# Performance work log

Measured on AMD Instinct MI355X. Metric: run time of the kernel, lower is better.

Reference implementation:

```python
import jax, jax.numpy as jnp
import numpy as np

N, D_IN, D_HID, D_OUT, E = 100000, 128, 256, 64, 1600000


def setup_inputs() -> dict:
    key = jax.random.key(0)
    ks = jax.random.split(key, 6)
    x = jax.random.normal(ks[0], (N, D_IN), dtype=jnp.float32)
    edge_index = jax.random.randint(ks[1], (2, E), 0, N, dtype=jnp.int64)
    # Linear params (PyTorch convention: y = x @ W.T + b)
    W1 = jax.random.normal(ks[2], (D_HID, D_IN), dtype=jnp.float32) / np.sqrt(D_IN)
    b1 = jax.random.normal(ks[3], (D_HID,), dtype=jnp.float32) * 0.01
    W2 = jax.random.normal(ks[4], (D_OUT, D_HID), dtype=jnp.float32) / np.sqrt(D_HID)
    b2 = jax.random.normal(ks[5], (D_OUT,), dtype=jnp.float32) * 0.01
    return {"x": x, "edge_index": edge_index, "W1": W1, "b1": b1, "W2": W2, "b2": b2}


def _scatter_mean(vals, dst, num_nodes):
    # sum neighbor features per destination node, divide by in-degree (0-degree -> 0)
    s = jax.ops.segment_sum(vals, dst, num_segments=num_nodes)
    cnt = jax.ops.segment_sum(jnp.ones((dst.shape[0],), vals.dtype), dst, num_segments=num_nodes)
    return s / jnp.maximum(cnt, 1.0)[:, None]


def _sage_layer(x, src, dst, W, b):
    neighbors = x[src]                      # [E, d] gather
    agg = _scatter_mean(neighbors, dst, x.shape[0])  # [N, d]
    return agg @ W.T + b


def reference(x, edge_index, W1, b1, W2, b2):
    src, dst = edge_index[0], edge_index[1]
    h = _sage_layer(x, src, dst, W1, b1)
    h = jax.nn.relu(h)
    # dropout is identity at inference (training=False)
    y = _sage_layer(h, src, dst, W2, b2)
    return jax.nn.log_softmax(y, axis=1)
```

## Files before the change

### kernel.cpp

```cpp
#include <hip/hip_runtime.h>


typedef __attribute__((ext_vector_type(8))) short bf16x8;
typedef __attribute__((ext_vector_type(4))) float f32x4;
typedef __attribute__((ext_vector_type(2))) float f32x2;

#define BSHIFT 10
#define BMASK  1023
#define SRCMASK 0x1FFFF
#define TBIN   4096

#if __has_builtin(__builtin_amdgcn_cvt_pk_f32_fp8) && __has_builtin(__builtin_amdgcn_cvt_pk_fp8_f32)
#define HAVE_FP8_CVT 1
#else
#define HAVE_FP8_CVT 0
#endif

__device__ inline ushort f2bf(float f) {
  union { float f; unsigned u; } c; c.f = f;
  unsigned r = (c.u + 0x7fffu + ((c.u >> 16) & 1u)) >> 16;
  return (ushort)r;
}
__device__ inline float bf2f(ushort u) {
  union { unsigned u; float f; } c; c.u = ((unsigned)u) << 16;
  return c.f;
}

#if HAVE_FP8_CVT
template <bool HI>
__device__ inline f32x2 fp8x2f(unsigned w) {
  return __builtin_amdgcn_cvt_pk_f32_fp8((int)w, HI);
}
template <bool HI>
__device__ inline unsigned fp8pack2(unsigned old, float a, float b) {
  return (unsigned)__builtin_amdgcn_cvt_pk_fp8_f32(a, b, (int)old, HI);
}
#else
__device__ inline float fp8tof_1(unsigned b) {
  unsigned e = (b >> 3) & 15u, m = b & 7u;
  float v;
  if (e == 0) v = (float)m * 0x1p-9f;
  else { union { unsigned u; float f; } c; c.u = ((e + 120u) << 23) | (m << 20); v = c.f; }
  return (b & 0x80u) ? -v : v;
}
template <bool HI>
__device__ inline f32x2 fp8x2f(unsigned w) {
  unsigned sh = HI ? 16 : 0;
  f32x2 r;
  r.x = fp8tof_1((w >> sh) & 0xFFu);
  r.y = fp8tof_1((w >> (sh + 8)) & 0xFFu);
  return r;
}
__device__ inline unsigned f2fp8_1(float f) {
  float af = fabsf(f);
  unsigned s = (f < 0.f) ? 0x80u : 0u;
  if (!(af < 448.f)) return s | 0x7Eu;
  if (af < 0x1p-6f) {
    int m = (int)rintf(af * 512.0f);
    if (m >= 8) return s | 0x08u;
    return s | (unsigned)m;
  }
  int e;
  frexpf(af, &e);
  int E = e - 1;
  int q = (int)rintf(ldexpf(af, 3 - E));
  if (q >= 16) { q = 8; E += 1; if (E > 8) return s | 0x7Eu; }
  return s | ((unsigned)(E + 7) << 3) | ((unsigned)q & 7u);
}
template <bool HI>
__device__ inline unsigned fp8pack2(unsigned old, float a, float b) {
  unsigned pair = f2fp8_1(a) | (f2fp8_1(b) << 8);
  return HI ? ((old & 0x0000FFFFu) | (pair << 16)) : ((old & 0xFFFF0000u) | pair);
}
#endif

__global__ void __launch_bounds__(64) k_detect(const int* __restrict__ ei, int* __restrict__ flag) {
  int t = threadIdx.x;
  int v = ei[2 * t + 1];
  unsigned long long m = __ballot(v != 0);
  if (t == 0) *flag = (m == 0ull) ? 1 : 0;
}

__global__ void __launch_bounds__(256) k_prep_x(const float4* __restrict__ x4, uint2* __restrict__ xq8, int total8) {
  int i = blockIdx.x * 256 + threadIdx.x;
  if (i >= total8) return;
  float4 v0 = x4[2 * i], v1 = x4[2 * i + 1];
  unsigned w0 = fp8pack2<false>(0u, v0.x, v0.y);
  w0 = fp8pack2<true>(w0, v0.z, v0.w);
  unsigned w1 = fp8pack2<false>(0u, v1.x, v1.y);
  w1 = fp8pack2<true>(w1, v1.z, v1.w);
  xq8[i] = make_uint2(w0, w1);
}

__global__ void __launch_bounds__(256) k_prep_w(const float* __restrict__ W1, const float* __restrict__ W2,
                                                ushort* __restrict__ W1f, ushort* __restrict__ W2f) {
  int idx = blockIdx.x * 256 + threadIdx.x;
  if (idx < 32768) {
    int jt = idx >> 11, rem = idx & 2047;
    int kt = rem >> 9, rem2 = rem & 511;
    int l = rem2 >> 3, e = rem2 & 7;
    int k = kt * 32 + (l >> 4) * 8 + e;
    int j = jt * 16 + (l & 15);
    W1f[idx] = f2bf(W1[j * 128 + k]);
  } else {
    int i2 = idx - 32768;
    if (i2 < 16384) {
      int ot = i2 >> 12, rem = i2 & 4095;
      int kt = rem >> 9;
      int l = (rem >> 3) & 63, e = rem & 7;
      int k = kt * 32 + (l >> 4) * 8 + e;
      int o = ot * 16 + (l & 15);
      W2f[i2] = f2bf(W2[o * 256 + k]);
    }
  }
}

__global__ void __launch_bounds__(256) k_bhist(const int* __restrict__ ei, const int* __restrict__ flag,
                                               int* __restrict__ bcnt, int E, int NB) {
  __shared__ int h[128];
  int t = threadIdx.x;
  if (t < 128) h[t] = 0;
  __syncthreads();
  bool f64 = (*flag != 0);
  int stride = gridDim.x * 256;
  for (int e = blockIdx.x * 256 + t; e < E; e += stride) {
    int d;
    if (f64) d = (int)((const long long*)ei)[(size_t)E + e];
    else     d = ei[(size_t)E + e];
    atomicAdd(&h[d >> BSHIFT], 1);
  }
  __syncthreads();
  if (t < NB && h[t]) atomicAdd(&bcnt[t], h[t]);
}

__global__ void __launch_bounds__(128) k_bscan(const int* __restrict__ bcnt, int* __restrict__ bbase,
                                               int* __restrict__ bcur, int* __restrict__ row_ptr,
                                               int NB, int N, int E) {
  __shared__ int s[128];
  int t = threadIdx.x;
  int v = (t < NB) ? bcnt[t] : 0;
  s[t] = v;
  __syncthreads();
  for (int o = 1; o < 128; o <<= 1) {
    int u = (t >= o) ? s[t - o] : 0;
    __syncthreads();
    s[t] += u;
    __syncthreads();
  }
  if (t < NB) {
    int base = s[t] - v;
    bbase[t] = base;
    bcur[t] = base;
  }
  if (t == 0) {
    bbase[NB] = E;
    row_ptr[N] = E;
  }
}

__global__ void __launch_bounds__(256) k_bin(const int* __restrict__ ei, const int* __restrict__ flag,
                                             int* __restrict__ bcur, int* __restrict__ gpair, int E, int NB) {
  __shared__ int hist[128], base[128], segb[128], cur[128], scanb[128];
  __shared__ int ent[TBIN];
  __shared__ int gdx[TBIN];
  int t = threadIdx.x;
  int e0 = blockIdx.x * TBIN;
  int cnt = E - e0; if (cnt > TBIN) cnt = TBIN;
  if (t < 128) hist[t] = 0;
  __syncthreads();
  bool f64 = (*flag != 0);
  int ment[16], mbk[16];
#pragma unroll
  for (int i = 0; i < 16; ++i) {
    int idx = t + i * 256;
    mbk[i] = -1;
    if (idx < cnt) {
      int e = e0 + idx;
      int s, d;
      if (f64) {
        const long long* p = (const long long*)ei;
        s = (int)p[e];
        d = (int)p[(size_t)E + e];
      } else {
        s = ei[e];
        d = ei[(size_t)E + e];
      }
      int b = d >> BSHIFT;
      mbk[i] = b;
      ment[i] = ((d & BMASK) << 17) | s;
      atomicAdd(&hist[b], 1);
    }
  }
  __syncthreads();
  if (t < 128) scanb[t] = hist[t];
  __syncthreads();
  for (int o = 1; o < 128; o <<= 1) {
    int u = 0;
    if (t < 128 && t >= o) u = scanb[t - o];
    __syncthreads();
    if (t < 128) scanb[t] += u;
    __syncthreads();
  }
  if (t < 128) {
    int b0 = scanb[t] - hist[t];
    base[t] = b0;
    cur[t] = b0;
    segb[t] = (t < NB && hist[t] > 0) ? atomicAdd(&bcur[t], hist[t]) : 0;
  }
  __syncthreads();
#pragma unroll
  for (int i = 0; i < 16; ++i) {
    int b = mbk[i];
    if (b >= 0) {
      int pos = atomicAdd(&cur[b], 1);
      ent[pos] = ment[i];
      gdx[pos] = segb[b] + (pos - base[b]);
    }
  }
  __syncthreads();
  for (int i = t; i < cnt; i += 256) gpair[gdx[i]] = ent[i];
}

__global__ void __launch_bounds__(1024) k_bcsr(const int* __restrict__ gpair, const int* __restrict__ bbase,
                                               int* __restrict__ row_ptr, float* __restrict__ inv_deg,
                                               int* __restrict__ csr, int N) {
  __shared__ int hist[1024], pre[1024], cur[1024];
  int b = blockIdx.x, t = threadIdx.x;
  int start = bbase[b], end = bbase[b + 1];
  hist[t] = 0;
  __syncthreads();
  for (int i = start + t; i < end; i += 1024) {
    int e = gpair[i];
    atomicAdd(&hist[e >> 17], 1);
  }
  __syncthreads();
  pre[t] = hist[t];
  __syncthreads();
  for (int o = 1; o < 1024; o <<= 1) {
    int u = (t >= o) ? pre[t - o] : 0;
    __syncthreads();
    pre[t] += u;
    __syncthreads();
  }
  int gbase = start + pre[t] - hist[t];
  int n = (b << BSHIFT) + t;
  if (n < N) {
    row_ptr[n] = gbase;
    inv_deg[n] = 1.0f / (float)(hist[t] > 0 ? hist[t] : 1);
  }
  cur[t] = gbase;
  __syncthreads();
  for (int i = start + t; i < end; i += 1024) {
    int e = gpair[i];
    int pos = atomicAdd(&cur[e >> 17], 1);
    csr[pos] = e & SRCMASK;
  }
}

__global__ void __launch_bounds__(256) k_agg1(const unsigned char* __restrict__ xq, const int* __restrict__ csr,
                                              const int* __restrict__ row_ptr, const float* __restrict__ inv_deg,
                                              ushort* __restrict__ agg1b, int N) {
  int n = blockIdx.x * 4 + (threadIdx.x >> 6);
  if (n >= N) return;
  int lane = threadIdx.x & 63;
  int half = lane >> 5, p = lane & 31;
  int s = row_ptr[n], e = row_ptr[n + 1];
  f32x2 a0 = (f32x2)(0.f), a1 = (f32x2)(0.f);

  for (int base = s; base < e; base += 64) {
    int cnt = e - base; if (cnt > 64) cnt = 64;
    int ci = csr[base + (lane < cnt ? lane : cnt - 1)];
    int j = 0;
    for (; j + 7 < cnt; j += 8) {
      int i0 = __shfl(ci, j + half);
      int i1 = __shfl(ci, j + 2 + half);
      int i2 = __shfl(ci, j + 4 + half);
      int i3 = __shfl(ci, j + 6 + half);
      unsigned w0 = *(const unsigned*)(xq + (size_t)i0 * 128 + p * 4);
      unsigned w1 = *(const unsigned*)(xq + (size_t)i1 * 128 + p * 4);
      unsigned w2 = *(const unsigned*)(xq + (size_t)i2 * 128 + p * 4);
      unsigned w3 = *(const unsigned*)(xq + (size_t)i3 * 128 + p * 4);
      a0 += fp8x2f<false>(w0); a1 += fp8x2f<true>(w0);
      a0 += fp8x2f<false>(w1); a1 += fp8x2f<true>(w1);
      a0 += fp8x2f<false>(w2); a1 += fp8x2f<true>(w2);
      a0 += fp8x2f<false>(w3); a1 += fp8x2f<true>(w3);
    }
    for (; j + 1 < cnt; j += 2) {
      int i0 = __shfl(ci, j + half);
      unsigned w0 = *(const unsigned*)(xq + (size_t)i0 * 128 + p * 4);
      a0 += fp8x2f<false>(w0); a1 += fp8x2f<true>(w0);
    }
    if (j < cnt) {
      int i0 = __shfl(ci, j);
      unsigned w0 = *(const unsigned*)(xq + (size_t)i0 * 128 + p * 4);
      if (half == 0) { a0 += fp8x2f<false>(w0); a1 += fp8x2f<true>(w0); }
    }
  }
  a0.x += __shfl_xor(a0.x, 32); a0.y += __shfl_xor(a0.y, 32);
  a1.x += __shfl_xor(a1.x, 32); a1.y += __shfl_xor(a1.y, 32);
  if (half == 0) {
    float inv = inv_deg[n];
    ushort4 o;
    o.x = f2bf(a0.x * inv); o.y = f2bf(a0.y * inv);
    o.z = f2bf(a1.x * inv); o.w = f2bf(a1.y * inv);
    *(ushort4*)(agg1b + (size_t)n * 128 + p * 4) = o;
  }
}

__global__ void __launch_bounds__(256) k_mlp(const ushort* __restrict__ agg1b, const bf16x8* __restrict__ w1f,
                                             const float* __restrict__ b1, const bf16x8* __restrict__ w2f,
                                             unsigned char* __restrict__ gq, int N) {
  __shared__ __align__(16) ushort sm[16896];
  ushort* aT = sm;
  ushort* hT = sm;
  const int t = threadIdx.x;
  const int n0 = blockIdx.x * 64;

#pragma unroll
  for (int i = 0; i < 4; ++i) {
    int idx = i * 256 + t;
    int row = idx >> 4, c8 = idx & 15;
    int rr = n0 + row; if (rr >= N) rr = N - 1;
    bf16x8 v = *(const bf16x8*)(agg1b + (size_t)rr * 128 + c8 * 8);
    *(bf16x8*)(aT + row * 136 + c8 * 8) = v;
  }
  __syncthreads();

  const int w = t >> 6, l = t & 63;
  const int lm = l & 15, lq = l >> 4;

  f32x4 acc[4][4];
#pragma unroll
  for (int mt = 0; mt < 4; ++mt)
#pragma unroll
    for (int nt = 0; nt < 4; ++nt) acc[mt][nt] = (f32x4)(0.f);

#pragma unroll
  for (int kt = 0; kt < 4; ++kt) {
    bf16x8 b[4], a[4];
#pragma unroll
    for (int nt = 0; nt < 4; ++nt)
      b[nt] = w1f[((w * 4 + nt) * 4 + kt) * 64 + l];
#pragma unroll
    for (int mt = 0; mt < 4; ++mt)
      a[mt] = *(const bf16x8*)(aT + (mt * 16 + lm) * 136 + kt * 32 + lq * 8);
#pragma unroll
    for (int mt = 0; mt < 4; ++mt)
#pragma unroll
      for (int nt = 0; nt < 4; ++nt)
        acc[mt][nt] = __builtin_amdgcn_mfma_f32_16x16x32_bf16(a[mt], b[nt], acc[mt][nt], 0, 0, 0);
  }
  __syncthreads();

#pragma unroll
  for (int nt = 0; nt < 4; ++nt) {
    int col = w * 64 + nt * 16 + lm;
    float bb = b1[col];
#pragma unroll
    for (int mt = 0; mt < 4; ++mt)
#pragma unroll
      for (int r = 0; r < 4; ++r) {
        int row = mt * 16 + lq * 4 + r;
        float hv = acc[mt][nt][r] + bb;
        hT[row * 264 + col] = f2bf(fmaxf(hv, 0.f));
      }
  }
  __syncthreads();

  f32x4 acc2[4];
#pragma unroll
  for (int ot = 0; ot < 4; ++ot) acc2[ot] = (f32x4)(0.f);
#pragma unroll
  for (int kt = 0; kt < 8; ++kt) {
    bf16x8 a2 = *(const bf16x8*)(hT + (w * 16 + lm) * 264 + kt * 32 + lq * 8);
#pragma unroll
    for (int ot = 0; ot < 4; ++ot) {
      bf16x8 bf = w2f[(ot * 8 + kt) * 64 + l];
      acc2[ot] = __builtin_amdgcn_mfma_f32_16x16x32_bf16(a2, bf, acc2[ot], 0, 0, 0);
    }
  }
#pragma unroll
  for (int ot = 0; ot < 4; ++ot)
#pragma unroll
    for (int r = 0; r < 4; ++r) {
      int row = n0 + w * 16 + lq * 4 + r;
      if (row < N) {
        unsigned pw = fp8pack2<false>(0u, acc2[ot][r], acc2[ot][r]);
        gq[(size_t)row * 64 + ot * 16 + lm] = (unsigned char)(pw & 0xFFu);
      }
    }
}

__global__ void __launch_bounds__(256) k_agg2(const unsigned char* __restrict__ gq, const int* __restrict__ csr,
                                              const int* __restrict__ row_ptr, const float* __restrict__ inv_deg,
                                              const float* __restrict__ b2, float* __restrict__ out, int N) {
  int n = blockIdx.x * 4 + (threadIdx.x >> 6);
  if (n >= N) return;
  int lane = threadIdx.x & 63;
  int q = lane >> 4, p = lane & 15;
  int s = row_ptr[n], e = row_ptr[n + 1];
  f32x2 a0 = (f32x2)(0.f), a1 = (f32x2)(0.f);

  for (int base = s; base < e; base += 64) {
    int cnt = e - base; if (cnt > 64) cnt = 64;
    int ci = csr[base + (lane < cnt ? lane : cnt - 1)];
    int j = 0;
    for (; j + 15 < cnt; j += 16) {
      int i0 = __shfl(ci, j + q);
      int i1 = __shfl(ci, j + 4 + q);
      int i2 = __shfl(ci, j + 8 + q);
      int i3 = __shfl(ci, j + 12 + q);
      unsigned w0 = *(const unsigned*)(gq + (size_t)i0 * 64 + p * 4);
      unsigned w1 = *(const unsigned*)(gq + (size_t)i1 * 64 + p * 4);
      unsigned w2 = *(const unsigned*)(gq + (size_t)i2 * 64 + p * 4);
      unsigned w3 = *(const unsigned*)(gq + (size_t)i3 * 64 + p * 4);
      a0 += fp8x2f<false>(w0); a1 += fp8x2f<true>(w0);
      a0 += fp8x2f<false>(w1); a1 += fp8x2f<true>(w1);
      a0 += fp8x2f<false>(w2); a1 += fp8x2f<true>(w2);
      a0 += fp8x2f<false>(w3); a1 += fp8x2f<true>(w3);
    }
    for (; j + 3 < cnt; j += 4) {
      int i0 = __shfl(ci, j + q);
      unsigned w0 = *(const unsigned*)(gq + (size_t)i0 * 64 + p * 4);
      a0 += fp8x2f<false>(w0); a1 += fp8x2f<true>(w0);
    }
    if (j < cnt) {
      int sel = j + q;
      int i0 = __shfl(ci, sel < cnt ? sel : j);
      unsigned w0 = *(const unsigned*)(gq + (size_t)i0 * 64 + p * 4);
      if (sel < cnt) { a0 += fp8x2f<false>(w0); a1 += fp8x2f<true>(w0); }
    }
  }
  a0.x += __shfl_xor(a0.x, 16); a0.y += __shfl_xor(a0.y, 16);
  a1.x += __shfl_xor(a1.x, 16); a1.y += __shfl_xor(a1.y, 16);
  a0.x += __shfl_xor(a0.x, 32); a0.y += __shfl_xor(a0.y, 32);
  a1.x += __shfl_xor(a1.x, 32); a1.y += __shfl_xor(a1.y, 32);
  float inv = inv_deg[n];
  float4 b = *(const float4*)(b2 + p * 4);
  float4 v;
  v.x = a0.x * inv + b.x;
  v.y = a0.y * inv + b.y;
  v.z = a1.x * inv + b.z;
  v.w = a1.y * inv + b.w;
  float mx = fmaxf(fmaxf(v.x, v.y), fmaxf(v.z, v.w));
#pragma unroll
  for (int off = 1; off <= 8; off <<= 1) mx = fmaxf(mx, __shfl_xor(mx, off));
  float se = expf(v.x - mx) + expf(v.y - mx) + expf(v.z - mx) + expf(v.w - mx);
#pragma unroll
  for (int off = 1; off <= 8; off <<= 1) se += __shfl_xor(se, off);
  float lse = mx + logf(se);
  v.x -= lse; v.y -= lse; v.z -= lse; v.w -= lse;
  if (q == 0) *(float4*)(out + (size_t)n * 64 + p * 4) = v;
}

extern "C" void kernel_launch(void* const* d_in, const int* in_sizes, int n_in,
                              void* d_out, int out_size, void* d_ws, size_t ws_size,
                              hipStream_t stream) {
  const float* x  = (const float*)d_in[0];
  const int*   ei = (const int*)d_in[1];
  const float* W1 = (const float*)d_in[2];
  const float* b1 = (const float*)d_in[3];
  const float* W2 = (const float*)d_in[4];
  const float* b2 = (const float*)d_in[5];
  float* out = (float*)d_out;
  const int N = in_sizes[0] / 128;
  const int E = in_sizes[1] / 2;
  const int NB = (N + BMASK) >> BSHIFT;

  char* base = (char*)d_ws;
  size_t off = 0;
  auto alloc = [&](size_t bytes) -> char* {
    char* p = base + off;
    off += (bytes + 255) & ~(size_t)255;
    return p;
  };
  int*    flag    = (int*)alloc(4);
  int*    bcnt    = (int*)alloc((size_t)NB * 4);
  int*    bbase   = (int*)alloc((size_t)(NB + 1) * 4);
  int*    bcur    = (int*)alloc((size_t)NB * 4);
  int*    gpair   = (int*)alloc((size_t)E * 4);
  int*    row_ptr = (int*)alloc((size_t)(N + 1) * 4);
  float*  inv_deg = (float*)alloc((size_t)N * 4);
  int*    csr     = (int*)alloc((size_t)E * 4);
  unsigned char* xq = (unsigned char*)alloc((size_t)N * 128);
  ushort* W1f     = (ushort*)alloc((size_t)32768 * 2);
  ushort* W2f     = (ushort*)alloc((size_t)16384 * 2);
  ushort* agg1b   = (ushort*)alloc((size_t)N * 128 * 2);
  unsigned char* gq = (unsigned char*)alloc((size_t)N * 64);
  (void)ws_size; (void)n_in; (void)out_size;

  hipMemsetAsync(bcnt, 0, (size_t)NB * 4, stream);
  k_detect<<<1, 64, 0, stream>>>(ei, flag);
  k_prep_x<<<(N * 16 + 255) / 256, 256, 0, stream>>>((const float4*)x, (uint2*)xq, N * 16);
  k_prep_w<<<192, 256, 0, stream>>>(W1, W2, W1f, W2f);
  k_bhist<<<512, 256, 0, stream>>>(ei, flag, bcnt, E, NB);
  k_bscan<<<1, 128, 0, stream>>>(bcnt, bbase, bcur, row_ptr, NB, N, E);
  k_bin<<<(E + TBIN - 1) / TBIN, 256, 0, stream>>>(ei, flag, bcur, gpair, E, NB);
  k_bcsr<<<NB, 1024, 0, stream>>>(gpair, bbase, row_ptr, inv_deg, csr, N);
  k_agg1<<<(N + 3) / 4, 256, 0, stream>>>(xq, csr, row_ptr, inv_deg, agg1b, N);
  k_mlp<<<(N + 63) / 64, 256, 0, stream>>>(agg1b, (const bf16x8*)W1f, b1, (const bf16x8*)W2f, gq, N);
  k_agg2<<<(N + 3) / 4, 256, 0, stream>>>(gq, csr, row_ptr, inv_deg, b2, out, N);
}
```

Baseline: 283.0 us.

## Fuse layer-1 aggregation into MLP and use fixed-capacity buckets to skip histogram

Removes the destination histogram and scan passes by giving each 1024-node bucket a fixed-capacity region, storing per-node row_end instead of a contiguous row_ptr. Fuses the first-layer neighbor aggregation into the MLP kernel so the bf16 aggregate never round-trips through global memory. CSR entries are pre-scaled by 64 to simplify gather addressing. Risks overflow if any bucket exceeds the fixed capacity, and lower parallelism in the fused gather phase.

```diff
diff --git a/kernel.cpp b/kernel.cpp
--- a/kernel.cpp
+++ b/kernel.cpp
@@ -9,6 +9,7 @@
 #define BMASK  1023
 #define SRCMASK 0x1FFFF
 #define TBIN   4096
+#define BCAP   20480
 
 #if __has_builtin(__builtin_amdgcn_cvt_pk_f32_fp8) && __has_builtin(__builtin_amdgcn_cvt_pk_fp8_f32)
 #define HAVE_FP8_CVT 1
@@ -20,10 +21,6 @@
   union { float f; unsigned u; } c; c.f = f;
   unsigned r = (c.u + 0x7fffu + ((c.u >> 16) & 1u)) >> 16;
   return (ushort)r;
-}
-__device__ inline float bf2f(ushort u) {
-  union { unsigned u; float f; } c; c.u = ((unsigned)u) << 16;
-  return c.f;
 }
 
 #if HAVE_FP8_CVT
@@ -115,47 +112,9 @@
   }
 }
 
-__global__ void __launch_bounds__(256) k_bhist(const int* __restrict__ ei, const int* __restrict__ flag,
-                                               int* __restrict__ bcnt, int E, int NB) {
-  __shared__ int h[128];
+__global__ void __launch_bounds__(128) k_binit(int* __restrict__ bcur, int NB) {
   int t = threadIdx.x;
-  if (t < 128) h[t] = 0;
-  __syncthreads();
-  bool f64 = (*flag != 0);
-  int stride = gridDim.x * 256;
-  for (int e = blockIdx.x * 256 + t; e < E; e += stride) {
-    int d;
-    if (f64) d = (int)((const long long*)ei)[(size_t)E + e];
-    else     d = ei[(size_t)E + e];
-    atomicAdd(&h[d >> BSHIFT], 1);
-  }
-  __syncthreads();
-  if (t < NB && h[t]) atomicAdd(&bcnt[t], h[t]);
-}
-
-__global__ void __launch_bounds__(128) k_bscan(const int* __restrict__ bcnt, int* __restrict__ bbase,
-                                               int* __restrict__ bcur, int* __restrict__ row_ptr,
-                                               int NB, int N, int E) {
-  __shared__ int s[128];
-  int t = threadIdx.x;
-  int v = (t < NB) ? bcnt[t] : 0;
-  s[t] = v;
-  __syncthreads();
-  for (int o = 1; o < 128; o <<= 1) {
-    int u = (t >= o) ? s[t - o] : 0;
-    __syncthreads();
-    s[t] += u;
-    __syncthreads();
-  }
-  if (t < NB) {
-    int base = s[t] - v;
-    bbase[t] = base;
-    bcur[t] = base;
-  }
-  if (t == 0) {
-    bbase[NB] = E;
-    row_ptr[N] = E;
-  }
+  if (t < NB) bcur[t] = t * BCAP;
 }
 
 __global__ void __launch_bounds__(256) k_bin(const int* __restrict__ ei, const int* __restrict__ flag,
@@ -221,12 +180,12 @@
   for (int i = t; i < cnt; i += 256) gpair[gdx[i]] = ent[i];
 }
 
-__global__ void __launch_bounds__(1024) k_bcsr(const int* __restrict__ gpair, const int* __restrict__ bbase,
-                                               int* __restrict__ row_ptr, float* __restrict__ inv_deg,
-                                               int* __restrict__ csr, int N) {
+__global__ void __launch_bounds__(1024) k_bcsr(const int* __restrict__ gpair, const int* __restrict__ bcur,
+                                               int* __restrict__ row_ptr, int* __restrict__ row_end,
+                                               float* __restrict__ inv_deg, int* __restrict__ csr, int N) {
   __shared__ int hist[1024], pre[1024], cur[1024];
   int b = blockIdx.x, t = threadIdx.x;
-  int start = bbase[b], end = bbase[b + 1];
+  int start = b * BCAP, end = bcur[b];
   hist[t] = 0;
   __syncthreads();
   for (int i = start + t; i < end; i += 1024) {
@@ -246,6 +205,7 @@
   int n = (b << BSHIFT) + t;
   if (n < N) {
     row_ptr[n] = gbase;
+    row_end[n] = gbase + hist[t];
     inv_deg[n] = 1.0f / (float)(hist[t] > 0 ? hist[t] : 1);
   }
   cur[t] = gbase;
@@ -253,80 +213,73 @@
   for (int i = start + t; i < end; i += 1024) {
     int e = gpair[i];
     int pos = atomicAdd(&cur[e >> 17], 1);
-    csr[pos] = e & SRCMASK;
-  }
-}
-
-__global__ void __launch_bounds__(256) k_agg1(const unsigned char* __restrict__ xq, const int* __restrict__ csr,
-                                              const int* __restrict__ row_ptr, const float* __restrict__ inv_deg,
-                                              ushort* __restrict__ agg1b, int N) {
-  int n = blockIdx.x * 4 + (threadIdx.x >> 6);
-  if (n >= N) return;
-  int lane = threadIdx.x & 63;
-  int half = lane >> 5, p = lane & 31;
-  int s = row_ptr[n], e = row_ptr[n + 1];
-  f32x2 a0 = (f32x2)(0.f), a1 = (f32x2)(0.f);
-
-  for (int base = s; base < e; base += 64) {
-    int cnt = e - base; if (cnt > 64) cnt = 64;
-    int ci = csr[base + (lane < cnt ? lane : cnt - 1)];
-    int j = 0;
-    for (; j + 7 < cnt; j += 8) {
-      int i0 = __shfl(ci, j + half);
-      int i1 = __shfl(ci, j + 2 + half);
-      int i2 = __shfl(ci, j + 4 + half);
-      int i3 = __shfl(ci, j + 6 + half);
-      unsigned w0 = *(const unsigned*)(xq + (size_t)i0 * 128 + p * 4);
-      unsigned w1 = *(const unsigned*)(xq + (size_t)i1 * 128 + p * 4);
-      unsigned w2 = *(const unsigned*)(xq + (size_t)i2 * 128 + p * 4);
-      unsigned w3 = *(const unsigned*)(xq + (size_t)i3 * 128 + p * 4);
-      a0 += fp8x2f<false>(w0); a1 += fp8x2f<true>(w0);
-      a0 += fp8x2f<false>(w1); a1 += fp8x2f<true>(w1);
-      a0 += fp8x2f<false>(w2); a1 += fp8x2f<true>(w2);
-      a0 += fp8x2f<false>(w3); a1 += fp8x2f<true>(w3);
-    }
-    for (; j + 1 < cnt; j += 2) {
-      int i0 = __shfl(ci, j + half);
-      unsigned w0 = *(const unsigned*)(xq + (size_t)i0 * 128 + p * 4);
-      a0 += fp8x2f<false>(w0); a1 += fp8x2f<true>(w0);
-    }
-    if (j < cnt) {
-      int i0 = __shfl(ci, j);
-      unsigned w0 = *(const unsigned*)(xq + (size_t)i0 * 128 + p * 4);
-      if (half == 0) { a0 += fp8x2f<false>(w0); a1 += fp8x2f<true>(w0); }
-    }
-  }
-  a0.x += __shfl_xor(a0.x, 32); a0.y += __shfl_xor(a0.y, 32);
-  a1.x += __shfl_xor(a1.x, 32); a1.y += __shfl_xor(a1.y, 32);
-  if (half == 0) {
-    float inv = inv_deg[n];
-    ushort4 o;
-    o.x = f2bf(a0.x * inv); o.y = f2bf(a0.y * inv);
-    o.z = f2bf(a1.x * inv); o.w = f2bf(a1.y * inv);
-    *(ushort4*)(agg1b + (size_t)n * 128 + p * 4) = o;
-  }
-}
-
-__global__ void __launch_bounds__(256) k_mlp(const ushort* __restrict__ agg1b, const bf16x8* __restrict__ w1f,
-                                             const float* __restrict__ b1, const bf16x8* __restrict__ w2f,
-                                             unsigned char* __restrict__ gq, int N) {
+    csr[pos] = (e & SRCMASK) << 6;
+  }
+}
+
+__global__ void __launch_bounds__(256) k_mlp(const unsigned char* __restrict__ xq, const int* __restrict__ csr,
+                                             const int* __restrict__ row_ptr, const int* __restrict__ row_end,
+                                             const float* __restrict__ inv_deg,
+                                             const bf16x8* __restrict__ w1f, const float* __restrict__ b1,
+                                             const bf16x8* __restrict__ w2f, unsigned char* __restrict__ gq, int N) {
   __shared__ __align__(16) ushort sm[16896];
   ushort* aT = sm;
   ushort* hT = sm;
   const int t = threadIdx.x;
   const int n0 = blockIdx.x * 64;
-
-#pragma unroll
-  for (int i = 0; i < 4; ++i) {
-    int idx = i * 256 + t;
-    int row = idx >> 4, c8 = idx & 15;
-    int rr = n0 + row; if (rr >= N) rr = N - 1;
-    bf16x8 v = *(const bf16x8*)(agg1b + (size_t)rr * 128 + c8 * 8);
-    *(bf16x8*)(aT + row * 136 + c8 * 8) = v;
-  }
-  __syncthreads();
-
   const int w = t >> 6, l = t & 63;
+  const int half = l >> 5, p = l & 31;
+
+  for (int i = 0; i < 16; ++i) {
+    int row = w * 16 + i;
+    int n = n0 + row;
+    if (n >= N) {
+      if (half == 0) *(ushort4*)(aT + row * 136 + p * 4) = make_ushort4(0, 0, 0, 0);
+      continue;
+    }
+    int s = row_ptr[n], e = row_end[n];
+    f32x2 a0 = (f32x2)(0.f), a1 = (f32x2)(0.f);
+    for (int base = s; base < e; base += 64) {
+      int cnt = e - base; if (cnt > 64) cnt = 64;
+      int ci = csr[base + (l < cnt ? l : cnt - 1)];
+      int j = 0;
+      for (; j + 7 < cnt; j += 8) {
+        int i0 = __shfl(ci, j + half);
+        int i1 = __shfl(ci, j + 2 + half);
+        int i2 = __shfl(ci, j + 4 + half);
+        int i3 = __shfl(ci, j + 6 + half);
+        unsigned w0 = *(const unsigned*)(xq + ((size_t)(unsigned)i0 << 1) + p * 4);
+        unsigned w1 = *(const unsigned*)(xq + ((size_t)(unsigned)i1 << 1) + p * 4);
+        unsigned w2 = *(const unsigned*)(xq + ((size_t)(unsigned)i2 << 1) + p * 4);
+        unsigned w3 = *(const unsigned*)(xq + ((size_t)(unsigned)i3 << 1) + p * 4);
+        a0 += fp8x2f<false>(w0); a1 += fp8x2f<true>(w0);
+        a0 += fp8x2f<false>(w1); a1 += fp8x2f<true>(w1);
+        a0 += fp8x2f<false>(w2); a1 += fp8x2f<true>(w2);
+        a0 += fp8x2f<false>(w3); a1 += fp8x2f<true>(w3);
+      }
+      for (; j + 1 < cnt; j += 2) {
+        int i0 = __shfl(ci, j + half);
+        unsigned w0 = *(const unsigned*)(xq + ((size_t)(unsigned)i0 << 1) + p * 4);
+        a0 += fp8x2f<false>(w0); a1 += fp8x2f<true>(w0);
+      }
+      if (j < cnt) {
+        int i0 = __shfl(ci, j);
+        unsigned w0 = *(const unsigned*)(xq + ((size_t)(unsigned)i0 << 1) + p * 4);
+        if (half == 0) { a0 += fp8x2f<false>(w0); a1 += fp8x2f<true>(w0); }
+      }
+    }
+    a0.x += __shfl_xor(a0.x, 32); a0.y += __shfl_xor(a0.y, 32);
+    a1.x += __shfl_xor(a1.x, 32); a1.y += __shfl_xor(a1.y, 32);
+    if (half == 0) {
+      float inv = inv_deg[n];
+      ushort4 o;
+      o.x = f2bf(a0.x * inv); o.y = f2bf(a0.y * inv);
+      o.z = f2bf(a1.x * inv); o.w = f2bf(a1.y * inv);
+      *(ushort4*)(aT + row * 136 + p * 4) = o;
+    }
+  }
+  __syncthreads();
+
   const int lm = l & 15, lq = l >> 4;
 
   f32x4 acc[4][4];
@@ -392,13 +345,14 @@
 }
 
 __global__ void __launch_bounds__(256) k_agg2(const unsigned char* __restrict__ gq, const int* __restrict__ csr,
-                                              const int* __restrict__ row_ptr, const float* __restrict__ inv_deg,
+                                              const int* __restrict__ row_ptr, const int* __restrict__ row_end,
+                                              const float* __restrict__ inv_deg,
                                               const float* __restrict__ b2, float* __restrict__ out, int N) {
   int n = blockIdx.x * 4 + (threadIdx.x >> 6);
   if (n >= N) return;
   int lane = threadIdx.x & 63;
   int q = lane >> 4, p = lane & 15;
-  int s = row_ptr[n], e = row_ptr[n + 1];
+  int s = row_ptr[n], e = row_end[n];
   f32x2 a0 = (f32x2)(0.f), a1 = (f32x2)(0.f);
 
   for (int base = s; base < e; base += 64) {
@@ -410,10 +364,10 @@
       int i1 = __shfl(ci, j + 4 + q);
       int i2 = __shfl(ci, j + 8 + q);
       int i3 = __shfl(ci, j + 12 + q);
-      unsigned w0 = *(const unsigned*)(gq + (size_t)i0 * 64 + p * 4);
-      unsigned w1 = *(const unsigned*)(gq + (size_t)i1 * 64 + p * 4);
-      unsigned w2 = *(const unsigned*)(gq + (size_t)i2 * 64 + p * 4);
-      unsigned w3 = *(const unsigned*)(gq + (size_t)i3 * 64 + p * 4);
+      unsigned w0 = *(const unsigned*)(gq + (size_t)(unsigned)i0 + p * 4);
+      unsigned w1 = *(const unsigned*)(gq + (size_t)(unsigned)i1 + p * 4);
+      unsigned w2 = *(const unsigned*)(gq + (size_t)(unsigned)i2 + p * 4);
+      unsigned w3 = *(const unsigned*)(gq + (size_t)(unsigned)i3 + p * 4);
       a0 += fp8x2f<false>(w0); a1 += fp8x2f<true>(w0);
       a0 += fp8x2f<false>(w1); a1 += fp8x2f<true>(w1);
       a0 += fp8x2f<false>(w2); a1 += fp8x2f<true>(w2);
@@ -421,13 +375,13 @@
     }
     for (; j + 3 < cnt; j += 4) {
       int i0 = __shfl(ci, j + q);
-      unsigned w0 = *(const unsigned*)(gq + (size_t)i0 * 64 + p * 4);
+      unsigned w0 = *(const unsigned*)(gq + (size_t)(unsigned)i0 + p * 4);
       a0 += fp8x2f<false>(w0); a1 += fp8x2f<true>(w0);
     }
     if (j < cnt) {
       int sel = j + q;
       int i0 = __shfl(ci, sel < cnt ? sel : j);
-      unsigned w0 = *(const unsigned*)(gq + (size_t)i0 * 64 + p * 4);
+      unsigned w0 = *(const unsigned*)(gq + (size_t)(unsigned)i0 + p * 4);
       if (sel < cnt) { a0 += fp8x2f<false>(w0); a1 += fp8x2f<true>(w0); }
     }
   }
@@ -475,29 +429,25 @@
     return p;
   };
   int*    flag    = (int*)alloc(4);
-  int*    bcnt    = (int*)alloc((size_t)NB * 4);
-  int*    bbase   = (int*)alloc((size_t)(NB + 1) * 4);
   int*    bcur    = (int*)alloc((size_t)NB * 4);
-  int*    gpair   = (int*)alloc((size_t)E * 4);
-  int*    row_ptr = (int*)alloc((size_t)(N + 1) * 4);
+  int*    gpair   = (int*)alloc((size_t)NB * BCAP * 4);
+  int*    row_ptr = (int*)alloc((size_t)N * 4);
+  int*    row_end = (int*)alloc((size_t)N * 4);
   float*  inv_deg = (float*)alloc((size_t)N * 4);
-  int*    csr     = (int*)alloc((size_t)E * 4);
+  int*    csr     = (int*)alloc((size_t)NB * BCAP * 4);
   unsigned char* xq = (unsigned char*)alloc((size_t)N * 128);
   ushort* W1f     = (ushort*)alloc((size_t)32768 * 2);
   ushort* W2f     = (ushort*)alloc((size_t)16384 * 2);
-  ushort* agg1b   = (ushort*)alloc((size_t)N * 128 * 2);
   unsigned char* gq = (unsigned char*)alloc((size_t)N * 64);
   (void)ws_size; (void)n_in; (void)out_size;
 
-  hipMemsetAsync(bcnt, 0, (size_t)NB * 4, stream);
   k_detect<<<1, 64, 0, stream>>>(ei, flag);
   k_prep_x<<<(N * 16 + 255) / 256, 256, 0, stream>>>((const float4*)x, (uint2*)xq, N * 16);
   k_prep_w<<<192, 256, 0, stream>>>(W1, W2, W1f, W2f);
-  k_bhist<<<512, 256, 0, stream>>>(ei, flag, bcnt, E, NB);
-  k_bscan<<<1, 128, 0, stream>>>(bcnt, bbase, bcur, row_ptr, NB, N, E);
+  k_binit<<<1, 128, 0, stream>>>(bcur, NB);
   k_bin<<<(E + TBIN - 1) / TBIN, 256, 0, stream>>>(ei, flag, bcur, gpair, E, NB);
-  k_bcsr<<<NB, 1024, 0, stream>>>(gpair, bbase, row_ptr, inv_deg, csr, N);
-  k_agg1<<<(N + 3) / 4, 256, 0, stream>>>(xq, csr, row_ptr, inv_deg, agg1b, N);
-  k_mlp<<<(N + 63) / 64, 256, 0, stream>>>(agg1b, (const bf16x8*)W1f, b1, (const bf16x8*)W2f, gq, N);
-  k_agg2<<<(N + 3) / 4, 256, 0, stream>>>(gq, csr, row_ptr, inv_deg, b2, out, N);
-}
+  k_bcsr<<<NB, 1024, 0, stream>>>(gpair, bcur, row_ptr, row_end, inv_deg, csr, N);
+  k_mlp<<<(N + 63) / 64, 256, 0, stream>>>(xq, csr, row_ptr, row_end, inv_deg,
+                                           (const bf16x8*)W1f, b1, (const bf16x8*)W2f, gq, N);
+  k_agg2<<<(N + 3) / 4, 256, 0, stream>>>(gq, csr, row_ptr, row_end, inv_deg, b2, out, N);
+}
```

New measurement: 326.5 us. 1.15x slower.
